# Kernel optimization log

Measured on AMD Instinct MI355X. Metric: run time of the kernel, lower is better.

Reference implementation:

```python
import jax, jax.numpy as jnp
import numpy as np

N, DEG, F_IN, H = 50000, 16, 128, 32
E = N * DEG


def _linear_params(key, out_f, in_f):
    kw, kb = jax.random.split(key)
    s = 1.0 / np.sqrt(in_f)
    W = jax.random.uniform(kw, (out_f, in_f), jnp.float32, -s, s)
    b = jax.random.uniform(kb, (out_f,), jnp.float32, -s, s)
    return W, b


def setup_inputs() -> dict:
    key = jax.random.key(0)
    ks = jax.random.split(key, 12)
    X = jax.random.normal(ks[0], (N, F_IN), jnp.float32)
    # DEG distinct nonzero offsets shared by all rows -> unique (src,dst) pairs,
    # so the COO tensor is already coalesced (no duplicate indices).
    offsets = jax.random.permutation(ks[1], jnp.arange(1, N))[:DEG]
    src = jnp.repeat(jnp.arange(N, dtype=jnp.int32), DEG)
    dst = ((src.reshape(N, DEG) + offsets[None, :].astype(jnp.int32)) % N).reshape(-1)
    D = jax.ops.segment_sum(jnp.ones((E,), jnp.float32), src, num_segments=N)
    wn1p, bn1p = _linear_params(ks[2], H, F_IN)      # convN1.pass_map
    wn1s, bn1s = _linear_params(ks[3], H, F_IN)      # convN1.self_map
    we1p, be1p = _linear_params(ks[4], H, 2 * H)     # convE1.pass_map
    we1s, be1s = _linear_params(ks[5], H, F_IN)      # convE1.self_map
    wn2p, bn2p = _linear_params(ks[6], H, H)         # convN2.pass_map
    wn2s, bn2s = _linear_params(ks[7], H, H)         # convN2.self_map
    we2p, be2p = _linear_params(ks[8], H, 2 * H)     # convE2.pass_map
    we2s, be2s = _linear_params(ks[9], H, H)         # convE2.self_map
    wc, bc = _linear_params(ks[10], 1, H)            # classifier
    return dict(X=X, src=src, dst=dst, D=D,
                wn1p=wn1p, bn1p=bn1p, wn1s=wn1s, bn1s=bn1s,
                we1p=we1p, be1p=be1p, we1s=we1s, be1s=be1s,
                wn2p=wn2p, bn2p=bn2p, wn2s=wn2s, bn2s=bn2s,
                we2p=we2p, be2p=be2p, we2s=we2s, be2s=be2s,
                wc=wc, bc=bc)


def reference(X, src, dst, D,
              wn1p, bn1p, wn1s, bn1s,
              we1p, be1p, we1s, be1s,
              wn2p, bn2p, wn2s, bn2s,
              we2p, be2p, we2s, be2s,
              wc, bc):
    n = X.shape[0]

    def node_conv(vals, Xn, wp, bp, ws, bs):
        # torch.sparse.sum(A, dim=1): sum edge values per source row
        Asum = jax.ops.segment_sum(vals, src, num_segments=n)
        return jax.nn.relu((Asum / D[:, None]) @ wp.T + bp + Xn @ ws.T + bs)

    def edge_conv(vals, Xn, wp, bp, ws, bs):
        X1, X2 = Xn[src], Xn[dst]
        Ef = jnp.concatenate([(X1 - X2) * 0.5, (X1 + X2) * 0.5], axis=-1)
        return jax.nn.relu(Ef @ wp.T + bp + vals @ ws.T + bs)

    # add_graph: edge features = |X[src] - X[dst]|
    vals0 = jnp.abs(X[src] - X[dst])            # (E, F_IN)
    X0 = jnp.zeros_like(X)                       # forward zeros node features
    Xn1 = node_conv(vals0, X0, wn1p, bn1p, wn1s, bn1s)   # (N, 32)
    vals1 = edge_conv(vals0, Xn1, we1p, be1p, we1s, be1s)  # (E, 32)
    Xn2 = node_conv(vals1, Xn1, wn2p, bn2p, wn2s, bn2s)  # (N, 32)
    vals2 = edge_conv(vals1, Xn2, we2p, be2p, we2s, be2s)  # (E, 32)
    SX = jax.nn.sigmoid(vals2 @ wc.T + bc)[:, 0]          # (E,)
    return SX
```

## Files before the change

kernel.cpp:

```cpp
#include <hip/hip_runtime.h>

#define DEG 16
#define F_IN 128
#define H 32

typedef __attribute__((ext_vector_type(8))) _Float16 f16x8;
typedef __attribute__((ext_vector_type(4))) float f32x4;
typedef __attribute__((ext_vector_type(4))) int i32x4;

union HS  { _Float16 f; unsigned short s; };
union HF4 { _Float16 h[4]; uint2 u; };

__device__ __forceinline__ float relu_f(float x) { return fmaxf(x, 0.0f); }

__device__ __forceinline__ f16x8 habs8(f16x8 a) {
    union { f16x8 h; i32x4 i; } u; u.h = a;
#pragma unroll
    for (int k = 0; k < 4; ++k) u.i[k] &= 0x7FFF7FFF;
    return u.h;
}

__global__ __launch_bounds__(256) void k_xhalf(
    const float* __restrict__ X, _Float16* __restrict__ Xh, long n8)
{
    const long t = (long)blockIdx.x * 256 + threadIdx.x;
    if (t >= n8) return;
    const float4* p = (const float4*)X + t * 2;
    const float4 a = p[0], b = p[1];
    f16x8 h;
    h[0] = (_Float16)a.x; h[1] = (_Float16)a.y; h[2] = (_Float16)a.z; h[3] = (_Float16)a.w;
    h[4] = (_Float16)b.x; h[5] = (_Float16)b.y; h[6] = (_Float16)b.z; h[7] = (_Float16)b.w;
    *(f16x8*)(Xh + t * 8) = h;
}

__global__ __launch_bounds__(256) void k_prep(
    const float* __restrict__ we1s, const float* __restrict__ we1p,
    const float* __restrict__ be1p, const float* __restrict__ be1s,
    const float* __restrict__ we2p, const float* __restrict__ we2s,
    const float* __restrict__ be2p, const float* __restrict__ be2s,
    const float* __restrict__ wn1p, const float* __restrict__ bn1p,
    const float* __restrict__ bn1s,
    const float* __restrict__ wn2p, const float* __restrict__ bn2p,
    const float* __restrict__ wn2s, const float* __restrict__ bn2s,
    _Float16* __restrict__ Wcat1, _Float16* __restrict__ Wcat2,
    _Float16* __restrict__ Wn1ph,
    _Float16* __restrict__ Wn2ph, _Float16* __restrict__ Wn2sh,
    float* __restrict__ bias1, float* __restrict__ bias2,
    float* __restrict__ biasn1, float* __restrict__ biasn2)
{
    const int t0 = blockIdx.x * 256 + threadIdx.x;
    const int stride = gridDim.x * 256;
    for (int idx = t0; idx < 32 * 192; idx += stride) {
        const int n = idx / 192, k = idx - n * 192;
        float w;
        if (k < 128)       w = we1s[n * 128 + k];
        else if (k < 160)  w = 0.5f * we1p[n * 64 + (k - 128)];
        else               w = 0.5f * we1p[n * 64 + 32 + (k - 160)];
        Wcat1[idx] = (_Float16)w;
    }
    for (int idx = t0; idx < 32 * 96; idx += stride) {
        const int n = idx / 96, k = idx - n * 96;
        float w;
        if (k < 32)       w = 0.5f * we2p[n * 64 + k];
        else if (k < 64)  w = 0.5f * we2p[n * 64 + 32 + (k - 32)];
        else              w = we2s[n * 32 + (k - 64)];
        Wcat2[idx] = (_Float16)w;
    }
    for (int idx = t0; idx < 32 * 128; idx += stride)
        Wn1ph[idx] = (_Float16)wn1p[idx];
    for (int idx = t0; idx < 32 * 32; idx += stride) {
        Wn2ph[idx] = (_Float16)wn2p[idx];
        Wn2sh[idx] = (_Float16)wn2s[idx];
    }
    if (t0 < H) {
        bias1[t0]  = be1p[t0] + be1s[t0];
        bias2[t0]  = be2p[t0] + be2s[t0];
        biasn1[t0] = bn1p[t0] + bn1s[t0];
        biasn2[t0] = bn2p[t0] + bn2s[t0];
    }
}

__global__ __launch_bounds__(256, 2) void k_p1(
    const _Float16* __restrict__ Xh, const int* __restrict__ dst,
    const float* __restrict__ D,
    const _Float16* __restrict__ Wcat1, const _Float16* __restrict__ Wn1ph,
    const float* __restrict__ biasn1,
    _Float16* __restrict__ t1h, _Float16* __restrict__ Xn1h, int N)
{
    const int wave = threadIdx.x >> 6;
    const int lane = threadIdx.x & 63;
    const int chunk = blockIdx.x * 4 + wave;
    const int i0 = chunk * 16;
    if (i0 >= N) return;
    const int m = lane & 15, g = lane >> 4;
    const int srow = (i0 + m < N) ? (i0 + m) : (N - 1);

    i32x4 dj4[4];
    {
        const i32x4* dp = (const i32x4*)(dst + (size_t)srow * DEG);
#pragma unroll
        for (int q = 0; q < 4; ++q) dj4[q] = dp[q];
    }
    f16x8 sv[4];
#pragma unroll
    for (int kb = 0; kb < 4; ++kb)
        sv[kb] = *(const f16x8*)(Xh + (size_t)srow * F_IN + kb * 32 + g * 8);
    f16x8 Bs[4][2], Bn[4][2];
#pragma unroll
    for (int kb = 0; kb < 4; ++kb)
#pragma unroll
        for (int t = 0; t < 2; ++t) {
            Bs[kb][t] = *(const f16x8*)(Wcat1 + (t * 16 + m) * 192 + kb * 32 + g * 8);
            Bn[kb][t] = *(const f16x8*)(Wn1ph + (t * 16 + m) * 128 + kb * 32 + g * 8);
        }

    f16x8 tvc[4], tvn[4];
#pragma unroll
    for (int kb = 0; kb < 4; ++kb)
        tvc[kb] = *(const f16x8*)(Xh + (size_t)dj4[0][0] * F_IN + kb * 32 + g * 8);

    f32x4 cn0 = {0.f,0.f,0.f,0.f}, cn1 = {0.f,0.f,0.f,0.f};
#pragma unroll
    for (int j = 0; j < 16; ++j) {
        if (j < 15) {
            const int dn = dj4[(j + 1) >> 2][(j + 1) & 3];
#pragma unroll
            for (int kb = 0; kb < 4; ++kb)
                tvn[kb] = *(const f16x8*)(Xh + (size_t)dn * F_IN + kb * 32 + g * 8);
        }
        f32x4 cs0 = {0.f,0.f,0.f,0.f}, cs1 = {0.f,0.f,0.f,0.f};
#pragma unroll
        for (int kb = 0; kb < 4; ++kb) {
            const f16x8 a = habs8(sv[kb] - tvc[kb]);
            cs0 = __builtin_amdgcn_mfma_f32_16x16x32_f16(a, Bs[kb][0], cs0, 0, 0, 0);
            cs1 = __builtin_amdgcn_mfma_f32_16x16x32_f16(a, Bs[kb][1], cs1, 0, 0, 0);
            cn0 = __builtin_amdgcn_mfma_f32_16x16x32_f16(a, Bn[kb][0], cn0, 0, 0, 0);
            cn1 = __builtin_amdgcn_mfma_f32_16x16x32_f16(a, Bn[kb][1], cn1, 0, 0, 0);
        }
        const size_t tb = ((size_t)chunk * 16 + j) * 512;
        HF4 a;
#pragma unroll
        for (int r = 0; r < 4; ++r) a.h[r] = (_Float16)cs0[r];
        *(uint2*)(t1h + tb + lane * 4) = a.u;
#pragma unroll
        for (int r = 0; r < 4; ++r) a.h[r] = (_Float16)cs1[r];
        *(uint2*)(t1h + tb + 256 + lane * 4) = a.u;
#pragma unroll
        for (int kb = 0; kb < 4; ++kb) tvc[kb] = tvn[kb];
    }
    const float bn0 = biasn1[m], bn1v = biasn1[16 + m];
#pragma unroll
    for (int r = 0; r < 4; ++r) {
        const int node = i0 + g * 4 + r;
        if (node < N) {
            const float invD = 1.0f / D[node];
            Xn1h[(size_t)node * H + m]      = (_Float16)relu_f(cn0[r] * invD + bn0);
            Xn1h[(size_t)node * H + 16 + m] = (_Float16)relu_f(cn1[r] * invD + bn1v);
        }
    }
}

__global__ __launch_bounds__(256, 2) void k_p2(
    const int* __restrict__ dst, const _Float16* __restrict__ Xn1h,
    const _Float16* __restrict__ Wcat1, const float* __restrict__ bias1,
    const _Float16* __restrict__ Wn2ph, const _Float16* __restrict__ Wn2sh,
    const float* __restrict__ biasn2, const float* __restrict__ D,
    _Float16* t1v1,
    _Float16* __restrict__ Xn2h, int N)
{
    __shared__ unsigned short RPall[4][16 * 40];
    const int wave = threadIdx.x >> 6;
    const int lane = threadIdx.x & 63;
    const int chunk = blockIdx.x * 4 + wave;
    const int i0 = chunk * 16;
    if (i0 >= N) return;
    unsigned short* RP = RPall[wave];
    const int m = lane & 15, g = lane >> 4;
    const int srow = (i0 + m < N) ? (i0 + m) : (N - 1);

    i32x4 dj4[4];
    {
        const i32x4* dp = (const i32x4*)(dst + (size_t)srow * DEG);
#pragma unroll
        for (int q = 0; q < 4; ++q) dj4[q] = dp[q];
    }
    const f16x8 x1 = *(const f16x8*)(Xn1h + (size_t)srow * H + g * 8);
    f16x8 Bf[2][2];
#pragma unroll
    for (int kb = 0; kb < 2; ++kb)
#pragma unroll
        for (int t = 0; t < 2; ++t)
            Bf[kb][t] = *(const f16x8*)(Wcat1 + (t * 16 + m) * 192 + (4 + kb) * 32 + g * 8);

    f16x8 x2b[2];
    uint2 u0b[2], u1b[2];
#pragma unroll
    for (int s = 0; s < 2; ++s) {
        const int dn = dj4[s >> 2][s & 3];
        x2b[s] = *(const f16x8*)(Xn1h + (size_t)dn * H + g * 8);
        const size_t tb = ((size_t)chunk * 16 + s) * 512;
        u0b[s] = *(const uint2*)(t1v1 + tb + lane * 4);
        u1b[s] = *(const uint2*)(t1v1 + tb + 256 + lane * 4);
    }
    const float b0 = bias1[m], b1v = bias1[16 + m];
    f32x4 sB0 = {0.f,0.f,0.f,0.f}, sB1 = {0.f,0.f,0.f,0.f};
    const int rr = lane >> 2, qq = lane & 3;
#pragma unroll
    for (int j = 0; j < 16; ++j) {
        const int s = j & 1;
        const f16x8 x2 = x2b[s];
        const uint2 u0 = u0b[s], u1 = u1b[s];
        if (j < 14) {
            const int dn = dj4[(j + 2) >> 2][(j + 2) & 3];
            x2b[s] = *(const f16x8*)(Xn1h + (size_t)dn * H + g * 8);
            const size_t tbn = ((size_t)chunk * 16 + j + 2) * 512;
            u0b[s] = *(const uint2*)(t1v1 + tbn + lane * 4);
            u1b[s] = *(const uint2*)(t1v1 + tbn + 256 + lane * 4);
        }
        f32x4 c0, c1;
        { HF4 a; a.u = u0;
#pragma unroll
          for (int r = 0; r < 4; ++r) c0[r] = (float)a.h[r];
          a.u = u1;
#pragma unroll
          for (int r = 0; r < 4; ++r) c1[r] = (float)a.h[r]; }
        const f16x8 ad = x1 - x2;
        const f16x8 aS = x1 + x2;
        c0 = __builtin_amdgcn_mfma_f32_16x16x32_f16(ad, Bf[0][0], c0, 0, 0, 0);
        c1 = __builtin_amdgcn_mfma_f32_16x16x32_f16(ad, Bf[0][1], c1, 0, 0, 0);
        c0 = __builtin_amdgcn_mfma_f32_16x16x32_f16(aS, Bf[1][0], c0, 0, 0, 0);
        c1 = __builtin_amdgcn_mfma_f32_16x16x32_f16(aS, Bf[1][1], c1, 0, 0, 0);
#pragma unroll
        for (int r = 0; r < 4; ++r) {
            const float v0 = relu_f(c0[r] + b0);
            const float v1 = relu_f(c1[r] + b1v);
            HS h0, h1; h0.f = (_Float16)v0; h1.f = (_Float16)v1;
            RP[(g * 4 + r) * 40 + m]      = h0.s;
            RP[(g * 4 + r) * 40 + 16 + m] = h1.s;
            sB0[r] += v0; sB1[r] += v1;
        }
        const size_t tb = ((size_t)chunk * 16 + j) * 512;
        const i32x4 v = *(const i32x4*)(RP + rr * 40 + qq * 8);
        *(i32x4*)(t1v1 + tb + rr * 32 + qq * 8) = v;
    }
    _Float16* RPh = (_Float16*)RP;
#pragma unroll
    for (int r = 0; r < 4; ++r) {
        const int node = i0 + g * 4 + r;
        const float invD = 1.0f / D[(node < N) ? node : (N - 1)];
        RPh[(g * 4 + r) * 40 + m]      = (_Float16)(sB0[r] * invD);
        RPh[(g * 4 + r) * 40 + 16 + m] = (_Float16)(sB1[r] * invD);
    }
    const f16x8 aF = *(const f16x8*)(RPh + m * 40 + g * 8);
    f16x8 Bp[2], Bs2[2];
#pragma unroll
    for (int t = 0; t < 2; ++t) {
        Bp[t]  = *(const f16x8*)(Wn2ph + (t * 16 + m) * H + g * 8);
        Bs2[t] = *(const f16x8*)(Wn2sh + (t * 16 + m) * H + g * 8);
    }
    f32x4 c0 = {0.f,0.f,0.f,0.f}, c1 = {0.f,0.f,0.f,0.f};
    c0 = __builtin_amdgcn_mfma_f32_16x16x32_f16(aF, Bp[0], c0, 0, 0, 0);
    c1 = __builtin_amdgcn_mfma_f32_16x16x32_f16(aF, Bp[1], c1, 0, 0, 0);
    c0 = __builtin_amdgcn_mfma_f32_16x16x32_f16(x1, Bs2[0], c0, 0, 0, 0);
    c1 = __builtin_amdgcn_mfma_f32_16x16x32_f16(x1, Bs2[1], c1, 0, 0, 0);
    const float bp0 = biasn2[m], bp1 = biasn2[16 + m];
#pragma unroll
    for (int r = 0; r < 4; ++r) {
        const int node = i0 + g * 4 + r;
        if (node < N) {
            Xn2h[(size_t)node * H + m]      = (_Float16)relu_f(c0[r] + bp0);
            Xn2h[(size_t)node * H + 16 + m] = (_Float16)relu_f(c1[r] + bp1);
        }
    }
}

__global__ __launch_bounds__(256, 2) void k_p3(
    const _Float16* __restrict__ Xn2h, const int* __restrict__ dst,
    const _Float16* __restrict__ vals1,
    const _Float16* __restrict__ Wcat2, const float* __restrict__ bias2,
    const float* __restrict__ wc, const float* __restrict__ bc,
    float* __restrict__ out, int N)
{
    __shared__ float outSall[4][16 * 16];
    const int wave = threadIdx.x >> 6;
    const int lane = threadIdx.x & 63;
    const int chunk = blockIdx.x * 4 + wave;
    const int i0 = chunk * 16;
    if (i0 >= N) return;
    float* outS = outSall[wave];
    const int m = lane & 15, g = lane >> 4;
    const int srow = (i0 + m < N) ? (i0 + m) : (N - 1);

    i32x4 dj4[4];
    {
        const i32x4* dp = (const i32x4*)(dst + (size_t)srow * DEG);
#pragma unroll
        for (int q = 0; q < 4; ++q) dj4[q] = dp[q];
    }
    const f16x8 x1 = *(const f16x8*)(Xn2h + (size_t)srow * H + g * 8);
    f16x8 Bf[3][2];
#pragma unroll
    for (int kb = 0; kb < 3; ++kb)
#pragma unroll
        for (int t = 0; t < 2; ++t)
            Bf[kb][t] = *(const f16x8*)(Wcat2 + (t * 16 + m) * 96 + kb * 32 + g * 8);

    f16x8 x2b[2], avb[2];
#pragma unroll
    for (int s = 0; s < 2; ++s) {
        const int dn = dj4[s >> 2][s & 3];
        x2b[s] = *(const f16x8*)(Xn2h + (size_t)dn * H + g * 8);
        avb[s] = *(const f16x8*)(vals1 + ((size_t)chunk * 16 + s) * 512 + m * 32 + g * 8);
    }
    const float b0 = bias2[m], b1v = bias2[16 + m];
    const float w0 = wc[m], w1 = wc[16 + m];
#pragma unroll
    for (int j = 0; j < 16; ++j) {
        const int s = j & 1;
        const f16x8 x2 = x2b[s];
        const f16x8 av = avb[s];
        if (j < 14) {
            const int dn = dj4[(j + 2) >> 2][(j + 2) & 3];
            x2b[s] = *(const f16x8*)(Xn2h + (size_t)dn * H + g * 8);
            avb[s] = *(const f16x8*)(vals1 + ((size_t)chunk * 16 + j + 2) * 512 + m * 32 + g * 8);
        }
        const f16x8 ad = x1 - x2;
        const f16x8 aS = x1 + x2;
        f32x4 c0 = {0.f,0.f,0.f,0.f}, c1 = {0.f,0.f,0.f,0.f};
        c0 = __builtin_amdgcn_mfma_f32_16x16x32_f16(ad, Bf[0][0], c0, 0, 0, 0);
        c1 = __builtin_amdgcn_mfma_f32_16x16x32_f16(ad, Bf[0][1], c1, 0, 0, 0);
        c0 = __builtin_amdgcn_mfma_f32_16x16x32_f16(aS, Bf[1][0], c0, 0, 0, 0);
        c1 = __builtin_amdgcn_mfma_f32_16x16x32_f16(aS, Bf[1][1], c1, 0, 0, 0);
        c0 = __builtin_amdgcn_mfma_f32_16x16x32_f16(av, Bf[2][0], c0, 0, 0, 0);
        c1 = __builtin_amdgcn_mfma_f32_16x16x32_f16(av, Bf[2][1], c1, 0, 0, 0);

        float sr[4];
#pragma unroll
        for (int r = 0; r < 4; ++r)
            sr[r] = relu_f(c0[r] + b0) * w0 + relu_f(c1[r] + b1v) * w1;
#pragma unroll
        for (int mask = 1; mask < 16; mask <<= 1) {
#pragma unroll
            for (int r = 0; r < 4; ++r)
                sr[r] += __shfl_xor(sr[r], mask);
        }
        if (m == 0) {
#pragma unroll
            for (int r = 0; r < 4; ++r)
                outS[(g * 4 + r) * 16 + j] = sr[r];
        }
    }
    {
        const float bcv = bc[0];
        const float* s = outS + lane * 4;
        float4 o;
        o.x = 1.0f / (1.0f + __expf(-(s[0] + bcv)));
        o.y = 1.0f / (1.0f + __expf(-(s[1] + bcv)));
        o.z = 1.0f / (1.0f + __expf(-(s[2] + bcv)));
        o.w = 1.0f / (1.0f + __expf(-(s[3] + bcv)));
        if (i0 + 16 <= N || (i0 + (lane >> 2)) < N)
            *(float4*)(out + (size_t)i0 * DEG + lane * 4) = o;
    }
}

extern "C" void kernel_launch(void* const* d_in, const int* in_sizes, int n_in,
                              void* d_out, int out_size, void* d_ws, size_t ws_size,
                              hipStream_t stream)
{
    const float* X    = (const float*)d_in[0];
    const int*   dst  = (const int*)  d_in[2];
    const float* D    = (const float*)d_in[3];
    const float* wn1p = (const float*)d_in[4];
    const float* bn1p = (const float*)d_in[5];
    const float* bn1s = (const float*)d_in[7];
    const float* we1p = (const float*)d_in[8];
    const float* be1p = (const float*)d_in[9];
    const float* we1s = (const float*)d_in[10];
    const float* be1s = (const float*)d_in[11];
    const float* wn2p = (const float*)d_in[12];
    const float* bn2p = (const float*)d_in[13];
    const float* wn2s = (const float*)d_in[14];
    const float* bn2s = (const float*)d_in[15];
    const float* we2p = (const float*)d_in[16];
    const float* be2p = (const float*)d_in[17];
    const float* we2s = (const float*)d_in[18];
    const float* be2s = (const float*)d_in[19];
    const float* wc   = (const float*)d_in[20];
    const float* bc   = (const float*)d_in[21];

    const int N = in_sizes[3];
    const int nbW = (N + 15) / 16;
    const int nbB = (nbW + 3) / 4;
    const size_t Epad = (size_t)nbW * 16 * DEG;

    char* w = (char*)d_ws;
    _Float16* t1v1  = (_Float16*)w;  w += Epad * H * 2;
    _Float16* Xh    = (_Float16*)w;  w += (size_t)N * F_IN * 2;
    _Float16* Xn1h  = (_Float16*)w;  w += (size_t)N * H * 2;
    _Float16* Xn2h  = (_Float16*)w;  w += (size_t)N * H * 2;
    _Float16* Wcat1 = (_Float16*)w;  w += 32 * 192 * 2;
    _Float16* Wcat2 = (_Float16*)w;  w += 32 * 96 * 2;
    _Float16* Wn1ph = (_Float16*)w;  w += 32 * 128 * 2;
    _Float16* Wn2ph = (_Float16*)w;  w += 32 * 32 * 2;
    _Float16* Wn2sh = (_Float16*)w;  w += 32 * 32 * 2;
    float* bias1  = (float*)w;       w += H * 4;
    float* bias2  = (float*)w;       w += H * 4;
    float* biasn1 = (float*)w;       w += H * 4;
    float* biasn2 = (float*)w;       w += H * 4;
    float* outp = (float*)d_out;

    const long n8 = (long)N * F_IN / 8;
    const int nbX = (int)((n8 + 255) / 256);

    k_xhalf<<<nbX, 256, 0, stream>>>(X, Xh, n8);
    k_prep<<<32, 256, 0, stream>>>(we1s, we1p, be1p, be1s, we2p, we2s, be2p, be2s,
                                   wn1p, bn1p, bn1s, wn2p, bn2p, wn2s, bn2s,
                                   Wcat1, Wcat2, Wn1ph, Wn2ph, Wn2sh,
                                   bias1, bias2, biasn1, biasn2);
    k_p1<<<nbB, 256, 0, stream>>>(Xh, dst, D, Wcat1, Wn1ph, biasn1, t1v1, Xn1h, N);
    k_p2<<<nbB, 256, 0, stream>>>(dst, Xn1h, Wcat1, bias1, Wn2ph, Wn2sh,
                                  biasn2, D, t1v1, Xn2h, N);
    k_p3<<<nbB, 256, 0, stream>>>(Xn2h, dst, t1v1, Wcat2, bias2, wc, bc, outp, N);
}
```

Baseline: 204.3 us.

## Fuse all stages into one persistent cooperative kernel with grid syncs

Replaces the five separate launches (fp16 conversion, weight prep, three graph stages) with one cooperative persistent kernel of 512 blocks. Each wave loops over 16-node chunks, and the stage boundaries become grid-wide barriers. This targets launch overhead and inter-kernel gaps, but adds grid-sync cost and fixes the grid size, which may limit occupancy and latency hiding compared to the full-size grids. A fallback path launches separate kernels with 64-thread blocks if the cooperative launch fails.

New measurement: 426.5 us. 2.09x slower.

```diff
diff --git a/kernel.cpp b/kernel.cpp
--- a/kernel.cpp
+++ b/kernel.cpp
@@ -1,4 +1,7 @@
 #include <hip/hip_runtime.h>
+#include <hip/hip_cooperative_groups.h>
+
+namespace cg = cooperative_groups;
 
 #define DEG 16
 #define F_IN 128
@@ -20,20 +23,20 @@
     return u.h;
 }
 
-__global__ __launch_bounds__(256) void k_xhalf(
+__device__ __forceinline__ void dev_xhalf(long t0, long stride,
     const float* __restrict__ X, _Float16* __restrict__ Xh, long n8)
 {
-    const long t = (long)blockIdx.x * 256 + threadIdx.x;
-    if (t >= n8) return;
-    const float4* p = (const float4*)X + t * 2;
-    const float4 a = p[0], b = p[1];
-    f16x8 h;
-    h[0] = (_Float16)a.x; h[1] = (_Float16)a.y; h[2] = (_Float16)a.z; h[3] = (_Float16)a.w;
-    h[4] = (_Float16)b.x; h[5] = (_Float16)b.y; h[6] = (_Float16)b.z; h[7] = (_Float16)b.w;
-    *(f16x8*)(Xh + t * 8) = h;
-}
-
-__global__ __launch_bounds__(256) void k_prep(
+    for (long t = t0; t < n8; t += stride) {
+        const float4* p = (const float4*)X + t * 2;
+        const float4 a = p[0], b = p[1];
+        f16x8 h;
+        h[0] = (_Float16)a.x; h[1] = (_Float16)a.y; h[2] = (_Float16)a.z; h[3] = (_Float16)a.w;
+        h[4] = (_Float16)b.x; h[5] = (_Float16)b.y; h[6] = (_Float16)b.z; h[7] = (_Float16)b.w;
+        *(f16x8*)(Xh + t * 8) = h;
+    }
+}
+
+__device__ __forceinline__ void dev_prep(int t0, int stride,
     const float* __restrict__ we1s, const float* __restrict__ we1p,
     const float* __restrict__ be1p, const float* __restrict__ be1s,
     const float* __restrict__ we2p, const float* __restrict__ we2s,
@@ -48,8 +51,6 @@
     float* __restrict__ bias1, float* __restrict__ bias2,
     float* __restrict__ biasn1, float* __restrict__ biasn2)
 {
-    const int t0 = blockIdx.x * 256 + threadIdx.x;
-    const int stride = gridDim.x * 256;
     for (int idx = t0; idx < 32 * 192; idx += stride) {
         const int n = idx / 192, k = idx - n * 192;
         float w;
@@ -80,18 +81,14 @@
     }
 }
 
-__global__ __launch_bounds__(256, 2) void k_p1(
+__device__ __forceinline__ void dev_p1(int chunk, int lane,
     const _Float16* __restrict__ Xh, const int* __restrict__ dst,
     const float* __restrict__ D,
     const _Float16* __restrict__ Wcat1, const _Float16* __restrict__ Wn1ph,
     const float* __restrict__ biasn1,
     _Float16* __restrict__ t1h, _Float16* __restrict__ Xn1h, int N)
 {
-    const int wave = threadIdx.x >> 6;
-    const int lane = threadIdx.x & 63;
-    const int chunk = blockIdx.x * 4 + wave;
     const int i0 = chunk * 16;
-    if (i0 >= N) return;
     const int m = lane & 15, g = lane >> 4;
     const int srow = (i0 + m < N) ? (i0 + m) : (N - 1);
 
@@ -160,21 +157,14 @@
     }
 }
 
-__global__ __launch_bounds__(256, 2) void k_p2(
+__device__ __forceinline__ void dev_p2(int chunk, int lane, unsigned short* RP,
     const int* __restrict__ dst, const _Float16* __restrict__ Xn1h,
     const _Float16* __restrict__ Wcat1, const float* __restrict__ bias1,
     const _Float16* __restrict__ Wn2ph, const _Float16* __restrict__ Wn2sh,
     const float* __restrict__ biasn2, const float* __restrict__ D,
-    _Float16* t1v1,
-    _Float16* __restrict__ Xn2h, int N)
-{
-    __shared__ unsigned short RPall[4][16 * 40];
-    const int wave = threadIdx.x >> 6;
-    const int lane = threadIdx.x & 63;
-    const int chunk = blockIdx.x * 4 + wave;
+    _Float16* t1v1, _Float16* __restrict__ Xn2h, int N)
+{
     const int i0 = chunk * 16;
-    if (i0 >= N) return;
-    unsigned short* RP = RPall[wave];
     const int m = lane & 15, g = lane >> 4;
     const int srow = (i0 + m < N) ? (i0 + m) : (N - 1);
 
@@ -274,20 +264,14 @@
     }
 }
 
-__global__ __launch_bounds__(256, 2) void k_p3(
+__device__ __forceinline__ void dev_p3(int chunk, int lane, float* outS,
     const _Float16* __restrict__ Xn2h, const int* __restrict__ dst,
     const _Float16* __restrict__ vals1,
     const _Float16* __restrict__ Wcat2, const float* __restrict__ bias2,
     const float* __restrict__ wc, const float* __restrict__ bc,
     float* __restrict__ out, int N)
 {
-    __shared__ float outSall[4][16 * 16];
-    const int wave = threadIdx.x >> 6;
-    const int lane = threadIdx.x & 63;
-    const int chunk = blockIdx.x * 4 + wave;
     const int i0 = chunk * 16;
-    if (i0 >= N) return;
-    float* outS = outSall[wave];
     const int m = lane & 15, g = lane >> 4;
     const int srow = (i0 + m < N) ? (i0 + m) : (N - 1);
 
@@ -361,6 +345,97 @@
         if (i0 + 16 <= N || (i0 + (lane >> 2)) < N)
             *(float4*)(out + (size_t)i0 * DEG + lane * 4) = o;
     }
+}
+
+__global__ __launch_bounds__(256, 3) void k_fused(
+    const float* X, const int* dst, const float* D,
+    const float* we1s, const float* we1p, const float* be1p, const float* be1s,
+    const float* we2p, const float* we2s, const float* be2p, const float* be2s,
+    const float* wn1p, const float* bn1p, const float* bn1s,
+    const float* wn2p, const float* bn2p, const float* wn2s, const float* bn2s,
+    const float* wc, const float* bc,
+    _Float16* Xh, _Float16* Wcat1, _Float16* Wcat2, _Float16* Wn1ph,
+    _Float16* Wn2ph, _Float16* Wn2sh,
+    float* bias1, float* bias2, float* biasn1, float* biasn2,
+    _Float16* t1v1, _Float16* Xn1h, _Float16* Xn2h, float* outp,
+    int N, int nbW, long n8)
+{
+    __shared__ unsigned short RPall[4][16 * 40];
+    __shared__ float outSall[4][16 * 16];
+    cg::grid_group gg = cg::this_grid();
+    const int wave = threadIdx.x >> 6;
+    const int lane = threadIdx.x & 63;
+    const int wid = blockIdx.x * 4 + wave;
+    const int WTOT = gridDim.x * 4;
+    const int t0 = blockIdx.x * 256 + threadIdx.x;
+    const int tstride = gridDim.x * 256;
+
+    dev_xhalf(t0, tstride, X, Xh, n8);
+    dev_prep(t0, tstride, we1s, we1p, be1p, be1s, we2p, we2s, be2p, be2s,
+             wn1p, bn1p, bn1s, wn2p, bn2p, wn2s, bn2s,
+             Wcat1, Wcat2, Wn1ph, Wn2ph, Wn2sh, bias1, bias2, biasn1, biasn2);
+    gg.sync();
+    for (int c = wid; c < nbW; c += WTOT)
+        dev_p1(c, lane, Xh, dst, D, Wcat1, Wn1ph, biasn1, t1v1, Xn1h, N);
+    gg.sync();
+    for (int c = wid; c < nbW; c += WTOT)
+        dev_p2(c, lane, RPall[wave], dst, Xn1h, Wcat1, bias1, Wn2ph, Wn2sh,
+               biasn2, D, t1v1, Xn2h, N);
+    gg.sync();
+    for (int c = wid; c < nbW; c += WTOT)
+        dev_p3(c, lane, outSall[wave], Xn2h, dst, t1v1, Wcat2, bias2, wc, bc,
+               outp, N);
+}
+
+__global__ __launch_bounds__(256) void k_xhalf(
+    const float* __restrict__ X, _Float16* __restrict__ Xh, long n8)
+{
+    dev_xhalf((long)blockIdx.x * 256 + threadIdx.x, (long)gridDim.x * 256, X, Xh, n8);
+}
+
+__global__ __launch_bounds__(256) void k_prep(
+    const float* we1s, const float* we1p, const float* be1p, const float* be1s,
+    const float* we2p, const float* we2s, const float* be2p, const float* be2s,
+    const float* wn1p, const float* bn1p, const float* bn1s,
+    const float* wn2p, const float* bn2p, const float* wn2s, const float* bn2s,
+    _Float16* Wcat1, _Float16* Wcat2, _Float16* Wn1ph,
+    _Float16* Wn2ph, _Float16* Wn2sh,
+    float* bias1, float* bias2, float* biasn1, float* biasn2)
+{
+    dev_prep(blockIdx.x * 256 + threadIdx.x, gridDim.x * 256,
+             we1s, we1p, be1p, be1s, we2p, we2s, be2p, be2s,
+             wn1p, bn1p, bn1s, wn2p, bn2p, wn2s, bn2s,
+             Wcat1, Wcat2, Wn1ph, Wn2ph, Wn2sh, bias1, bias2, biasn1, biasn2);
+}
+
+__global__ __launch_bounds__(64, 3) void k_p1s(
+    const _Float16* Xh, const int* dst, const float* D,
+    const _Float16* Wcat1, const _Float16* Wn1ph, const float* biasn1,
+    _Float16* t1h, _Float16* Xn1h, int N)
+{
+    dev_p1(blockIdx.x, threadIdx.x, Xh, dst, D, Wcat1, Wn1ph, biasn1, t1h, Xn1h, N);
+}
+
+__global__ __launch_bounds__(64, 4) void k_p2s(
+    const int* dst, const _Float16* Xn1h,
+    const _Float16* Wcat1, const float* bias1,
+    const _Float16* Wn2ph, const _Float16* Wn2sh,
+    const float* biasn2, const float* D,
+    _Float16* t1v1, _Float16* Xn2h, int N)
+{
+    __shared__ unsigned short RP[16 * 40];
+    dev_p2(blockIdx.x, threadIdx.x, RP, dst, Xn1h, Wcat1, bias1, Wn2ph, Wn2sh,
+           biasn2, D, t1v1, Xn2h, N);
+}
+
+__global__ __launch_bounds__(64, 4) void k_p3s(
+    const _Float16* Xn2h, const int* dst, const _Float16* vals1,
+    const _Float16* Wcat2, const float* bias2,
+    const float* wc, const float* bc, float* out, int N)
+{
+    __shared__ float outS[16 * 16];
+    dev_p3(blockIdx.x, threadIdx.x, outS, Xn2h, dst, vals1, Wcat2, bias2,
+           wc, bc, out, N);
 }
 
 extern "C" void kernel_launch(void* const* d_in, const int* in_sizes, int n_in,
@@ -390,7 +465,6 @@
 
     const int N = in_sizes[3];
     const int nbW = (N + 15) / 16;
-    const int nbB = (nbW + 3) / 4;
     const size_t Epad = (size_t)nbW * 16 * DEG;
 
     char* w = (char*)d_ws;
@@ -409,16 +483,34 @@
     float* biasn2 = (float*)w;       w += H * 4;
     float* outp = (float*)d_out;
 
-    const long n8 = (long)N * F_IN / 8;
-    const int nbX = (int)((n8 + 255) / 256);
-
-    k_xhalf<<<nbX, 256, 0, stream>>>(X, Xh, n8);
-    k_prep<<<32, 256, 0, stream>>>(we1s, we1p, be1p, be1s, we2p, we2s, be2p, be2s,
-                                   wn1p, bn1p, bn1s, wn2p, bn2p, wn2s, bn2s,
-                                   Wcat1, Wcat2, Wn1ph, Wn2ph, Wn2sh,
-                                   bias1, bias2, biasn1, biasn2);
-    k_p1<<<nbB, 256, 0, stream>>>(Xh, dst, D, Wcat1, Wn1ph, biasn1, t1v1, Xn1h, N);
-    k_p2<<<nbB, 256, 0, stream>>>(dst, Xn1h, Wcat1, bias1, Wn2ph, Wn2sh,
-                                  biasn2, D, t1v1, Xn2h, N);
-    k_p3<<<nbB, 256, 0, stream>>>(Xn2h, dst, t1v1, Wcat2, bias2, wc, bc, outp, N);
-}
+    long n8 = (long)N * F_IN / 8;
+    int Ni = N, nbWi = nbW;
+
+    void* args[] = {
+        (void*)&X, (void*)&dst, (void*)&D,
+        (void*)&we1s, (void*)&we1p, (void*)&be1p, (void*)&be1s,
+        (void*)&we2p, (void*)&we2s, (void*)&be2p, (void*)&be2s,
+        (void*)&wn1p, (void*)&bn1p, (void*)&bn1s,
+        (void*)&wn2p, (void*)&bn2p, (void*)&wn2s, (void*)&bn2s,
+        (void*)&wc, (void*)&bc,
+        (void*)&Xh, (void*)&Wcat1, (void*)&Wcat2, (void*)&Wn1ph,
+        (void*)&Wn2ph, (void*)&Wn2sh,
+        (void*)&bias1, (void*)&bias2, (void*)&biasn1, (void*)&biasn2,
+        (void*)&t1v1, (void*)&Xn1h, (void*)&Xn2h, (void*)&outp,
+        (void*)&Ni, (void*)&nbWi, (void*)&n8
+    };
+    hipError_t e = hipLaunchCooperativeKernel((void*)k_fused, dim3(512), dim3(256),
+                                              args, 0, stream);
+    if (e != hipSuccess) {
+        const int nbX = (int)((n8 + 255) / 256);
+        k_xhalf<<<nbX, 256, 0, stream>>>(X, Xh, n8);
+        k_prep<<<32, 256, 0, stream>>>(we1s, we1p, be1p, be1s, we2p, we2s, be2p, be2s,
+                                       wn1p, bn1p, bn1s, wn2p, bn2p, wn2s, bn2s,
+                                       Wcat1, Wcat2, Wn1ph, Wn2ph, Wn2sh,
+                                       bias1, bias2, biasn1, biasn2);
+        k_p1s<<<nbW, 64, 0, stream>>>(Xh, dst, D, Wcat1, Wn1ph, biasn1, t1v1, Xn1h, N);
+        k_p2s<<<nbW, 64, 0, stream>>>(dst, Xn1h, Wcat1, bias1, Wn2ph, Wn2sh,
+                                      biasn2, D, t1v1, Xn2h, N);
+        k_p3s<<<nbW, 64, 0, stream>>>(Xn2h, dst, t1v1, Wcat2, bias2, wc, bc, outp, N);
+    }
+}
```
